# Kernel tuning notes

Hardware: AMD Instinct MI355X
Metric: run time of the kernel (lower is better)

Reference implementation:

```python
import jax, jax.numpy as jnp
import numpy as np

DIM = 512
HEADS = 8
DIM_HEAD = 64
INNER = HEADS * DIM_HEAD  # 512
EPS = 1e-6


def setup_inputs() -> dict:
    key = jax.random.key(0)
    ks = jax.random.split(key, 6)
    B, N = 8, 2048
    x = jax.random.normal(ks[0], (B, N, DIM), dtype=jnp.float32)
    # nn.Linear stores weight as [out, in]; we keep that layout and transpose in matmul.
    w_qkv = jax.random.normal(ks[1], (3 * INNER, DIM), dtype=jnp.float32) * (1.0 / np.sqrt(DIM))
    w_proj = jax.random.normal(ks[2], (DIM, INNER), dtype=jnp.float32) * (1.0 / np.sqrt(INNER))
    b_proj = jax.random.normal(ks[3], (DIM,), dtype=jnp.float32) * 0.01
    ln_gamma = jnp.ones((DIM,), dtype=jnp.float32)
    ln_beta = jnp.zeros((DIM,), dtype=jnp.float32)
    return {"x": x, "w_qkv": w_qkv, "w_proj": w_proj, "b_proj": b_proj,
            "ln_gamma": ln_gamma, "ln_beta": ln_beta}


def reference(x, w_qkv, w_proj, b_proj, ln_gamma, ln_beta):
    B, N, D = x.shape
    H, Dh = HEADS, DIM_HEAD
    # LayerNorm (eps=1e-6)
    mu = jnp.mean(x, axis=-1, keepdims=True)
    var = jnp.mean(jnp.square(x - mu), axis=-1, keepdims=True)
    xn = (x - mu) * jax.lax.rsqrt(var + EPS) * ln_gamma + ln_beta
    # QKV projection (no bias)
    qkv = xn @ w_qkv.T  # [B, N, 3*INNER]
    q, k, v = jnp.split(qkv, 3, axis=-1)
    # [B, N, H, Dh] -> [B, H, N, Dh]
    q = q.reshape(B, N, H, Dh).transpose(0, 2, 1, 3)
    k = k.reshape(B, N, H, Dh).transpose(0, 2, 1, 3)
    v = v.reshape(B, N, H, Dh).transpose(0, 2, 1, 3)
    scale = Dh ** (-0.5)
    attn = jnp.einsum('bhnd,bhmd->bhnm', q, k) * scale  # [B, H, N, N]
    attn = jax.nn.softmax(attn, axis=-1)
    out = jnp.einsum('bhnm,bhmd->bhnd', attn, v)  # [B, H, N, Dh]
    out = out.transpose(0, 2, 1, 3).reshape(B, N, H * Dh)
    out = out @ w_proj.T + b_proj
    return out
```

## Files before the change

### kernel.cpp

```cpp
#include <hip/hip_runtime.h>

typedef unsigned short u16;
typedef __bf16 bf16x8 __attribute__((ext_vector_type(8)));
typedef float f32x4 __attribute__((ext_vector_type(4)));

#define DIMD 512
#define SEQN 2048
#define NB   8
#define NH   8
#define DH   64
#define BHN  (NB*NH)
#define MROWS (NB*SEQN)
#define QSCALE 0.18033688f

__device__ __forceinline__ u16 f2bf(float f) {
  union { float f; unsigned u; } x; x.f = f;
  unsigned r = x.u + 0x7fffu + ((x.u >> 16) & 1u);
  return (u16)(r >> 16);
}
__device__ __forceinline__ u16 f2bf_fast(float f) {
  union { float f; unsigned u; } x; x.f = f;
  return (u16)((x.u + 0x8000u) >> 16);
}

__device__ __forceinline__ void gll16(const u16* g, u16* lbase) {
#if __has_builtin(__builtin_amdgcn_global_load_lds)
  __builtin_amdgcn_global_load_lds(
      (const __attribute__((address_space(1))) unsigned int*)g,
      (__attribute__((address_space(3))) unsigned int*)lbase, 16, 0, 0);
#else
  *(uint4*)((u16*)lbase + (threadIdx.x & 63) * 8) = *(const uint4*)g;
#endif
}

__global__ __launch_bounds__(256) void wcvt2(
    const float* __restrict__ wa, const float* __restrict__ wb,
    u16* __restrict__ oa, u16* __restrict__ ob, int na, int nb) {
  int i = (blockIdx.x * 256 + threadIdx.x) * 8;
  const float* src; u16* dst; int idx;
  if (i < na) { src = wa; dst = oa; idx = i; }
  else { idx = i - na; if (idx >= nb) return; src = wb; dst = ob; }
  float4 f0 = *(const float4*)(src + idx);
  float4 f1 = *(const float4*)(src + idx + 4);
  union { uint4 v; u16 s[8]; } u;
  u.s[0] = f2bf(f0.x); u.s[1] = f2bf(f0.y); u.s[2] = f2bf(f0.z); u.s[3] = f2bf(f0.w);
  u.s[4] = f2bf(f1.x); u.s[5] = f2bf(f1.y); u.s[6] = f2bf(f1.z); u.s[7] = f2bf(f1.w);
  *(uint4*)(dst + idx) = u.v;
}

__global__ __launch_bounds__(256) void ln_kernel(
    const float* __restrict__ x, const float* __restrict__ gamma,
    const float* __restrict__ beta, u16* __restrict__ xn) {
  int row = blockIdx.x * 4 + (threadIdx.x >> 6);
  int lane = threadIdx.x & 63;
  const float* xr = x + (size_t)row * DIMD;
  float f[8], g[8], b[8];
  *(float4*)&f[0] = *(const float4*)(xr + lane * 8);
  *(float4*)&f[4] = *(const float4*)(xr + lane * 8 + 4);
  *(float4*)&g[0] = *(const float4*)(gamma + lane * 8);
  *(float4*)&g[4] = *(const float4*)(gamma + lane * 8 + 4);
  *(float4*)&b[0] = *(const float4*)(beta + lane * 8);
  *(float4*)&b[4] = *(const float4*)(beta + lane * 8 + 4);
  float sum = 0.f, sq = 0.f;
#pragma unroll
  for (int i = 0; i < 8; ++i) { sum += f[i]; sq += f[i] * f[i]; }
#pragma unroll
  for (int off = 1; off < 64; off <<= 1) {
    sum += __shfl_xor(sum, off, 64);
    sq  += __shfl_xor(sq, off, 64);
  }
  float mean = sum * (1.0f / DIMD);
  float var = sq * (1.0f / DIMD) - mean * mean;
  float rstd = rsqrtf(var + 1e-6f);
  union { uint4 v; u16 s[8]; } uo;
#pragma unroll
  for (int i = 0; i < 8; ++i)
    uo.s[i] = f2bf((f[i] - mean) * rstd * g[i] + b[i]);
  *(uint4*)(xn + (size_t)row * DIMD + lane * 8) = uo.v;
}

__global__ __launch_bounds__(256) void qkv_gemm(
    const u16* __restrict__ A, const u16* __restrict__ Bm,
    u16* __restrict__ qo, u16* __restrict__ ko, u16* __restrict__ vto) {
  __shared__ __align__(16) u16 la[128 * 32];
  __shared__ __align__(16) u16 lb[128 * 32];
  const int K = DIMD;
  int tid = threadIdx.x;
  int bm = blockIdx.x, bn = blockIdx.y;
  int wid = tid >> 6, lane = tid & 63, lm = lane & 15, quad = lane >> 4;
  int wm = wid >> 1, wn = wid & 1;
  f32x4 acc[4][4] = {};
  const u16* Ab = A + (size_t)(bm * 128) * K;
  const u16* Bb = Bm + (size_t)(bn * 128) * K;
  int srow = (lane >> 2), scol = (lane & 3) * 8;
  for (int k0 = 0; k0 < K; k0 += 32) {
    __syncthreads();
#pragma unroll
    for (int r = 0; r < 2; ++r) {
      int seg = wid * 2 + r;
      int row = seg * 16 + srow;
      gll16(Ab + (size_t)row * K + k0 + scol, &la[seg * 512]);
      gll16(Bb + (size_t)row * K + k0 + scol, &lb[seg * 512]);
    }
    __syncthreads();
    bf16x8 af[4], bfr[4];
#pragma unroll
    for (int i = 0; i < 4; ++i)
      af[i] = *(const bf16x8*)&la[(wm * 64 + i * 16 + lm) * 32 + quad * 8];
#pragma unroll
    for (int j = 0; j < 4; ++j)
      bfr[j] = *(const bf16x8*)&lb[(wn * 64 + j * 16 + lm) * 32 + quad * 8];
#pragma unroll
    for (int i = 0; i < 4; ++i)
#pragma unroll
      for (int j = 0; j < 4; ++j)
        acc[i][j] = __builtin_amdgcn_mfma_f32_16x16x32_bf16(af[i], bfr[j], acc[i][j], 0, 0, 0);
  }
  int part = bn >> 2;
  if (part == 2) {
#pragma unroll
    for (int i = 0; i < 4; ++i)
#pragma unroll
      for (int j = 0; j < 4; ++j) {
        int col = bn * 128 + wn * 64 + j * 16 + lm;
        int rem = col & 511, h = rem >> 6, d = rem & 63;
        int rg = bm * 128 + wm * 64 + i * 16 + quad * 4;
        int b = rg >> 11, nn = rg & 2047;
        union { unsigned long long ll; u16 s4[4]; } pk;
#pragma unroll
        for (int r = 0; r < 4; ++r) pk.s4[r] = f2bf(acc[i][j][r]);
        *(unsigned long long*)&vto[((size_t)(b * NH + h) * DH + d) * SEQN + nn] = pk.ll;
      }
  } else {
    u16* dst = part ? ko : qo;
    float sc = part ? 1.0f : QSCALE;
#pragma unroll
    for (int i = 0; i < 4; ++i)
#pragma unroll
      for (int j = 0; j < 4; ++j) {
        int col = bn * 128 + wn * 64 + j * 16 + lm;
        int rem = col & 511, h = rem >> 6, d = rem & 63;
#pragma unroll
        for (int r = 0; r < 4; ++r) {
          int rg = bm * 128 + wm * 64 + i * 16 + quad * 4 + r;
          int b = rg >> 11, nn = rg & 2047;
          dst[((size_t)(b * NH + h) * SEQN + nn) * DH + d] = f2bf(acc[i][j][r] * sc);
        }
      }
  }
}

__global__ __launch_bounds__(256, 4) void attn_kernel(
    const u16* __restrict__ q, const u16* __restrict__ k,
    const u16* __restrict__ vt, u16* __restrict__ att) {
  __shared__ __align__(16) u16 kt[2][64 * 64];
  __shared__ __align__(16) u16 vtt[2][64 * 64];
  __shared__ __align__(16) u16 plds[4 * 16 * 64];
  int bh = blockIdx.x;
  int wid = threadIdx.x >> 6, lane = threadIdx.x & 63;
  int lm = lane & 15, quad = lane >> 4;
  int qrow0 = blockIdx.y * 128 + wid * 32;
  const u16* qb = q + (size_t)bh * SEQN * DH;
  const u16* kb = k + (size_t)bh * SEQN * DH;
  const u16* vb = vt + (size_t)bh * DH * SEQN;
  u16* pw = plds + wid * (16 * 64);

  int cb_row = lane >> 3, cb_sub = lane & 7;
  int xsw = quad ^ (lm & 7);
  int lsw = lm & 7;

  bf16x8 ones;
#pragma unroll
  for (int i = 0; i < 8; ++i) ones[i] = (__bf16)1.0f;

  bf16x8 qf[2][2];
#pragma unroll
  for (int g = 0; g < 2; ++g)
#pragma unroll
    for (int c = 0; c < 2; ++c)
      qf[g][c] = *(const bf16x8*)(qb + (size_t)(qrow0 + g * 16 + lm) * DH + c * 32 + quad * 8);

  f32x4 Ot[2][4] = {};
  f32x4 lacc[2] = {};

  auto stage = [&](int bsel, int j0) {
    if (wid < 2) {
#pragma unroll
      for (int i = 0; i < 4; ++i) {
        int row = wid * 32 + i * 8 + cb_row;
        int sc = (cb_sub ^ (row & 7)) * 8;
        gll16(kb + (size_t)(j0 + row) * DH + sc, &kt[bsel][wid * 2048 + i * 512]);
      }
    } else {
#pragma unroll
      for (int i = 0; i < 4; ++i) {
        int row = (wid - 2) * 32 + i * 8 + cb_row;
        int sc = (cb_sub ^ (row & 7)) * 8;
        gll16(vb + (size_t)row * SEQN + j0 + sc, &vtt[bsel][(wid - 2) * 2048 + i * 512]);
      }
    }
  };

  stage(0, 0);
  for (int t = 0; t < SEQN / 64; ++t) {
    int bsel = t & 1;
    __syncthreads();
    if (t + 1 < SEQN / 64) stage(bsel ^ 1, (t + 1) * 64);

    bf16x8 kf[4][2];
#pragma unroll
    for (int js = 0; js < 4; ++js) {
      int row = js * 16 + lm;
      kf[js][0] = *(const bf16x8*)&kt[bsel][row * 64 + xsw * 8];
      kf[js][1] = *(const bf16x8*)&kt[bsel][row * 64 + (xsw ^ 4) * 8];
    }
    bf16x8 pa[2][2];
#pragma unroll
    for (int g = 0; g < 2; ++g) {
#pragma unroll
      for (int js = 0; js < 4; ++js) {
        f32x4 z = {0.f, 0.f, 0.f, 0.f};
        z = __builtin_amdgcn_mfma_f32_16x16x32_bf16(kf[js][0], qf[g][0], z, 0, 0, 0);
        z = __builtin_amdgcn_mfma_f32_16x16x32_bf16(kf[js][1], qf[g][1], z, 0, 0, 0);
        union { unsigned long long ll; u16 s4[4]; } pk;
#pragma unroll
        for (int r = 0; r < 4; ++r)
          pk.s4[r] = f2bf_fast(__builtin_amdgcn_exp2f(z[r]));
        int wc = (js * 2 + (quad >> 1)) ^ lsw;
        *(unsigned long long*)&pw[lm * 64 + wc * 8 + (quad & 1) * 4] = pk.ll;
      }
      pa[g][0] = *(const bf16x8*)&pw[lm * 64 + (quad ^ lsw) * 8];
      pa[g][1] = *(const bf16x8*)&pw[lm * 64 + ((4 + quad) ^ lsw) * 8];
      lacc[g] = __builtin_amdgcn_mfma_f32_16x16x32_bf16(ones, pa[g][0], lacc[g], 0, 0, 0);
      lacc[g] = __builtin_amdgcn_mfma_f32_16x16x32_bf16(ones, pa[g][1], lacc[g], 0, 0, 0);
    }
#pragma unroll
    for (int db = 0; db < 4; ++db) {
      int row = db * 16 + lm;
      bf16x8 va0 = *(const bf16x8*)&vtt[bsel][row * 64 + xsw * 8];
      bf16x8 va1 = *(const bf16x8*)&vtt[bsel][row * 64 + (xsw ^ 4) * 8];
      Ot[0][db] = __builtin_amdgcn_mfma_f32_16x16x32_bf16(va0, pa[0][0], Ot[0][db], 0, 0, 0);
      Ot[0][db] = __builtin_amdgcn_mfma_f32_16x16x32_bf16(va1, pa[0][1], Ot[0][db], 0, 0, 0);
      Ot[1][db] = __builtin_amdgcn_mfma_f32_16x16x32_bf16(va0, pa[1][0], Ot[1][db], 0, 0, 0);
      Ot[1][db] = __builtin_amdgcn_mfma_f32_16x16x32_bf16(va1, pa[1][1], Ot[1][db], 0, 0, 0);
    }
  }
  int b = bh >> 3, h = bh & 7;
#pragma unroll
  for (int g = 0; g < 2; ++g) {
    float inv = 1.0f / lacc[g][0];
    size_t rowoff = ((size_t)(b * SEQN + qrow0 + g * 16 + lm)) * DIMD + h * DH;
#pragma unroll
    for (int db = 0; db < 4; ++db) {
      union { unsigned long long ll; u16 s4[4]; } ok;
#pragma unroll
      for (int r = 0; r < 4; ++r) ok.s4[r] = f2bf(Ot[g][db][r] * inv);
      *(unsigned long long*)&att[rowoff + db * 16 + quad * 4] = ok.ll;
    }
  }
}

__global__ __launch_bounds__(256) void proj_gemm(
    const u16* __restrict__ A, const u16* __restrict__ Bm,
    const float* __restrict__ bias, float* __restrict__ C) {
  __shared__ __align__(16) u16 la[128 * 32];
  __shared__ __align__(16) u16 lb[128 * 32];
  const int K = DIMD, N = DIMD;
  int tid = threadIdx.x;
  int bm = blockIdx.x, bn = blockIdx.y;
  int wid = tid >> 6, lane = tid & 63, lm = lane & 15, quad = lane >> 4;
  int wm = wid >> 1, wn = wid & 1;
  f32x4 acc[4][4] = {};
  const u16* Ab = A + (size_t)(bm * 128) * K;
  const u16* Bb = Bm + (size_t)(bn * 128) * K;
  int srow = (lane >> 2), scol = (lane & 3) * 8;
  for (int k0 = 0; k0 < K; k0 += 32) {
    __syncthreads();
#pragma unroll
    for (int r = 0; r < 2; ++r) {
      int seg = wid * 2 + r;
      int row = seg * 16 + srow;
      gll16(Ab + (size_t)row * K + k0 + scol, &la[seg * 512]);
      gll16(Bb + (size_t)row * K + k0 + scol, &lb[seg * 512]);
    }
    __syncthreads();
    bf16x8 af[4], bfr[4];
#pragma unroll
    for (int i = 0; i < 4; ++i)
      af[i] = *(const bf16x8*)&la[(wm * 64 + i * 16 + lm) * 32 + quad * 8];
#pragma unroll
    for (int j = 0; j < 4; ++j)
      bfr[j] = *(const bf16x8*)&lb[(wn * 64 + j * 16 + lm) * 32 + quad * 8];
#pragma unroll
    for (int i = 0; i < 4; ++i)
#pragma unroll
      for (int j = 0; j < 4; ++j)
        acc[i][j] = __builtin_amdgcn_mfma_f32_16x16x32_bf16(af[i], bfr[j], acc[i][j], 0, 0, 0);
  }
#pragma unroll
  for (int i = 0; i < 4; ++i)
#pragma unroll
    for (int j = 0; j < 4; ++j) {
      int col = bn * 128 + wn * 64 + j * 16 + lm;
      float bv = bias[col];
#pragma unroll
      for (int r = 0; r < 4; ++r) {
        int rg = bm * 128 + wm * 64 + i * 16 + quad * 4 + r;
        C[(size_t)rg * N + col] = acc[i][j][r] + bv;
      }
    }
}

extern "C" void kernel_launch(void* const* d_in, const int* in_sizes, int n_in,
                              void* d_out, int out_size, void* d_ws, size_t ws_size,
                              hipStream_t stream) {
  const float* x      = (const float*)d_in[0];
  const float* w_qkv  = (const float*)d_in[1];
  const float* w_proj = (const float*)d_in[2];
  const float* b_proj = (const float*)d_in[3];
  const float* gamma  = (const float*)d_in[4];
  const float* beta   = (const float*)d_in[5];
  float* out = (float*)d_out;

  const size_t SZ = (size_t)MROWS * DIMD;
  u16* xn  = (u16*)d_ws;
  u16* q   = xn + SZ;
  u16* kk  = q + SZ;
  u16* vt  = kk + SZ;
  u16* wqb = vt + SZ;
  u16* wpb = wqb + (size_t)3 * DIMD * DIMD;
  u16* att = xn;

  const int NQKV = 3 * DIMD * DIMD;
  const int NPRJ = DIMD * DIMD;
  wcvt2<<<dim3((NQKV + NPRJ) / 2048), dim3(256), 0, stream>>>(
      w_qkv, w_proj, wqb, wpb, NQKV, NPRJ);
  ln_kernel<<<dim3(MROWS / 4), dim3(256), 0, stream>>>(x, gamma, beta, xn);
  qkv_gemm<<<dim3(MROWS / 128, (3 * DIMD) / 128), dim3(256), 0, stream>>>(
      xn, wqb, q, kk, vt);
  attn_kernel<<<dim3(BHN, SEQN / 128), dim3(256), 0, stream>>>(q, kk, vt, att);
  proj_gemm<<<dim3(MROWS / 128, DIMD / 128), dim3(256), 0, stream>>>(
      att, wpb, b_proj, out);
}
```

Before: 233.0 us.

## Use BK=64 swizzled LDS tiles in GEMMs and 8-wave attention blocks

The QKV and projection GEMMs now stage K-tiles of 64 instead of 32, with an XOR swizzle on the LDS layout. This halves the number of barrier pairs per K loop and is meant to avoid LDS bank conflicts. The attention kernel moves to 512-thread blocks covering 256 query rows, so each staged K/V tile is reused by twice as many waves. The cost is more LDS per block and possibly lower occupancy from the larger blocks and launch bounds.

```diff
diff --git a/kernel.cpp b/kernel.cpp
--- a/kernel.cpp
+++ b/kernel.cpp
@@ -82,39 +82,45 @@
 __global__ __launch_bounds__(256) void qkv_gemm(
     const u16* __restrict__ A, const u16* __restrict__ Bm,
     u16* __restrict__ qo, u16* __restrict__ ko, u16* __restrict__ vto) {
-  __shared__ __align__(16) u16 la[128 * 32];
-  __shared__ __align__(16) u16 lb[128 * 32];
+  __shared__ __align__(16) u16 la[128 * 64];
+  __shared__ __align__(16) u16 lb[128 * 64];
   const int K = DIMD;
   int tid = threadIdx.x;
   int bm = blockIdx.x, bn = blockIdx.y;
   int wid = tid >> 6, lane = tid & 63, lm = lane & 15, quad = lane >> 4;
   int wm = wid >> 1, wn = wid & 1;
+  int lsw = lm & 7;
   f32x4 acc[4][4] = {};
   const u16* Ab = A + (size_t)(bm * 128) * K;
   const u16* Bb = Bm + (size_t)(bn * 128) * K;
-  int srow = (lane >> 2), scol = (lane & 3) * 8;
-  for (int k0 = 0; k0 < K; k0 += 32) {
-    __syncthreads();
-#pragma unroll
-    for (int r = 0; r < 2; ++r) {
-      int seg = wid * 2 + r;
-      int row = seg * 16 + srow;
-      gll16(Ab + (size_t)row * K + k0 + scol, &la[seg * 512]);
-      gll16(Bb + (size_t)row * K + k0 + scol, &lb[seg * 512]);
-    }
-    __syncthreads();
-    bf16x8 af[4], bfr[4];
-#pragma unroll
-    for (int i = 0; i < 4; ++i)
-      af[i] = *(const bf16x8*)&la[(wm * 64 + i * 16 + lm) * 32 + quad * 8];
-#pragma unroll
-    for (int j = 0; j < 4; ++j)
-      bfr[j] = *(const bf16x8*)&lb[(wn * 64 + j * 16 + lm) * 32 + quad * 8];
-#pragma unroll
-    for (int i = 0; i < 4; ++i)
+  int cb_row = lane >> 3, cb_sub = lane & 7;
+  int xsrc = (cb_sub ^ cb_row) * 8;
+  for (int k0 = 0; k0 < K; k0 += 64) {
+    __syncthreads();
+#pragma unroll
+    for (int r = 0; r < 4; ++r) {
+      int seg = wid * 4 + r;
+      int row = seg * 8 + cb_row;
+      size_t goff = (size_t)row * K + k0 + xsrc;
+      gll16(Ab + goff, &la[seg * 512]);
+      gll16(Bb + goff, &lb[seg * 512]);
+    }
+    __syncthreads();
+#pragma unroll
+    for (int h = 0; h < 2; ++h) {
+      bf16x8 af[4], bfr[4];
+#pragma unroll
+      for (int i = 0; i < 4; ++i)
+        af[i] = *(const bf16x8*)&la[(wm * 64 + i * 16 + lm) * 64 + (((h * 4 + quad) ^ lsw) * 8)];
 #pragma unroll
       for (int j = 0; j < 4; ++j)
-        acc[i][j] = __builtin_amdgcn_mfma_f32_16x16x32_bf16(af[i], bfr[j], acc[i][j], 0, 0, 0);
+        bfr[j] = *(const bf16x8*)&lb[(wn * 64 + j * 16 + lm) * 64 + (((h * 4 + quad) ^ lsw) * 8)];
+#pragma unroll
+      for (int i = 0; i < 4; ++i)
+#pragma unroll
+        for (int j = 0; j < 4; ++j)
+          acc[i][j] = __builtin_amdgcn_mfma_f32_16x16x32_bf16(af[i], bfr[j], acc[i][j], 0, 0, 0);
+    }
   }
   int part = bn >> 2;
   if (part == 2) {
@@ -150,22 +156,23 @@
   }
 }
 
-__global__ __launch_bounds__(256, 4) void attn_kernel(
+__global__ __launch_bounds__(512, 4) void attn_kernel(
     const u16* __restrict__ q, const u16* __restrict__ k,
     const u16* __restrict__ vt, u16* __restrict__ att) {
   __shared__ __align__(16) u16 kt[2][64 * 64];
   __shared__ __align__(16) u16 vtt[2][64 * 64];
-  __shared__ __align__(16) u16 plds[4 * 16 * 64];
+  __shared__ __align__(16) u16 plds[8 * 16 * 64];
   int bh = blockIdx.x;
   int wid = threadIdx.x >> 6, lane = threadIdx.x & 63;
   int lm = lane & 15, quad = lane >> 4;
-  int qrow0 = blockIdx.y * 128 + wid * 32;
+  int qrow0 = blockIdx.y * 256 + wid * 32;
   const u16* qb = q + (size_t)bh * SEQN * DH;
   const u16* kb = k + (size_t)bh * SEQN * DH;
   const u16* vb = vt + (size_t)bh * DH * SEQN;
   u16* pw = plds + wid * (16 * 64);
 
   int cb_row = lane >> 3, cb_sub = lane & 7;
+  int xstage = (cb_sub ^ cb_row) * 8;
   int xsw = quad ^ (lm & 7);
   int lsw = lm & 7;
 
@@ -184,19 +191,19 @@
   f32x4 lacc[2] = {};
 
   auto stage = [&](int bsel, int j0) {
-    if (wid < 2) {
-#pragma unroll
-      for (int i = 0; i < 4; ++i) {
-        int row = wid * 32 + i * 8 + cb_row;
-        int sc = (cb_sub ^ (row & 7)) * 8;
-        gll16(kb + (size_t)(j0 + row) * DH + sc, &kt[bsel][wid * 2048 + i * 512]);
+    if (wid < 4) {
+#pragma unroll
+      for (int i = 0; i < 2; ++i) {
+        int seg = wid * 2 + i;
+        int row = seg * 8 + cb_row;
+        gll16(kb + (size_t)(j0 + row) * DH + xstage, &kt[bsel][seg * 512]);
       }
     } else {
 #pragma unroll
-      for (int i = 0; i < 4; ++i) {
-        int row = (wid - 2) * 32 + i * 8 + cb_row;
-        int sc = (cb_sub ^ (row & 7)) * 8;
-        gll16(vb + (size_t)row * SEQN + j0 + sc, &vtt[bsel][(wid - 2) * 2048 + i * 512]);
+      for (int i = 0; i < 2; ++i) {
+        int seg = (wid - 4) * 2 + i;
+        int row = seg * 8 + cb_row;
+        gll16(vb + (size_t)row * SEQN + j0 + xstage, &vtt[bsel][seg * 512]);
       }
     }
   };
@@ -263,39 +270,45 @@
 __global__ __launch_bounds__(256) void proj_gemm(
     const u16* __restrict__ A, const u16* __restrict__ Bm,
     const float* __restrict__ bias, float* __restrict__ C) {
-  __shared__ __align__(16) u16 la[128 * 32];
-  __shared__ __align__(16) u16 lb[128 * 32];
+  __shared__ __align__(16) u16 la[128 * 64];
+  __shared__ __align__(16) u16 lb[128 * 64];
   const int K = DIMD, N = DIMD;
   int tid = threadIdx.x;
   int bm = blockIdx.x, bn = blockIdx.y;
   int wid = tid >> 6, lane = tid & 63, lm = lane & 15, quad = lane >> 4;
   int wm = wid >> 1, wn = wid & 1;
+  int lsw = lm & 7;
   f32x4 acc[4][4] = {};
   const u16* Ab = A + (size_t)(bm * 128) * K;
   const u16* Bb = Bm + (size_t)(bn * 128) * K;
-  int srow = (lane >> 2), scol = (lane & 3) * 8;
-  for (int k0 = 0; k0 < K; k0 += 32) {
-    __syncthreads();
-#pragma unroll
-    for (int r = 0; r < 2; ++r) {
-      int seg = wid * 2 + r;
-      int row = seg * 16 + srow;
-      gll16(Ab + (size_t)row * K + k0 + scol, &la[seg * 512]);
-      gll16(Bb + (size_t)row * K + k0 + scol, &lb[seg * 512]);
-    }
-    __syncthreads();
-    bf16x8 af[4], bfr[4];
-#pragma unroll
-    for (int i = 0; i < 4; ++i)
-      af[i] = *(const bf16x8*)&la[(wm * 64 + i * 16 + lm) * 32 + quad * 8];
-#pragma unroll
-    for (int j = 0; j < 4; ++j)
-      bfr[j] = *(const bf16x8*)&lb[(wn * 64 + j * 16 + lm) * 32 + quad * 8];
-#pragma unroll
-    for (int i = 0; i < 4; ++i)
+  int cb_row = lane >> 3, cb_sub = lane & 7;
+  int xsrc = (cb_sub ^ cb_row) * 8;
+  for (int k0 = 0; k0 < K; k0 += 64) {
+    __syncthreads();
+#pragma unroll
+    for (int r = 0; r < 4; ++r) {
+      int seg = wid * 4 + r;
+      int row = seg * 8 + cb_row;
+      size_t goff = (size_t)row * K + k0 + xsrc;
+      gll16(Ab + goff, &la[seg * 512]);
+      gll16(Bb + goff, &lb[seg * 512]);
+    }
+    __syncthreads();
+#pragma unroll
+    for (int h = 0; h < 2; ++h) {
+      bf16x8 af[4], bfr[4];
+#pragma unroll
+      for (int i = 0; i < 4; ++i)
+        af[i] = *(const bf16x8*)&la[(wm * 64 + i * 16 + lm) * 64 + (((h * 4 + quad) ^ lsw) * 8)];
 #pragma unroll
       for (int j = 0; j < 4; ++j)
-        acc[i][j] = __builtin_amdgcn_mfma_f32_16x16x32_bf16(af[i], bfr[j], acc[i][j], 0, 0, 0);
+        bfr[j] = *(const bf16x8*)&lb[(wn * 64 + j * 16 + lm) * 64 + (((h * 4 + quad) ^ lsw) * 8)];
+#pragma unroll
+      for (int i = 0; i < 4; ++i)
+#pragma unroll
+        for (int j = 0; j < 4; ++j)
+          acc[i][j] = __builtin_amdgcn_mfma_f32_16x16x32_bf16(af[i], bfr[j], acc[i][j], 0, 0, 0);
+    }
   }
 #pragma unroll
   for (int i = 0; i < 4; ++i)
@@ -338,7 +351,7 @@
   ln_kernel<<<dim3(MROWS / 4), dim3(256), 0, stream>>>(x, gamma, beta, xn);
   qkv_gemm<<<dim3(MROWS / 128, (3 * DIMD) / 128), dim3(256), 0, stream>>>(
       xn, wqb, q, kk, vt);
-  attn_kernel<<<dim3(BHN, SEQN / 128), dim3(256), 0, stream>>>(q, kk, vt, att);
+  attn_kernel<<<dim3(BHN, SEQN / 256), dim3(512), 0, stream>>>(q, kk, vt, att);
   proj_gemm<<<dim3(MROWS / 128, DIMD / 128), dim3(256), 0, stream>>>(
       att, wpb, b_proj, out);
 }
```

New measurement: 220.7 us. -5.3%, faster.
